# Performance work log

Measured on AMD Instinct MI355X. Metric: run time of the kernel, lower is better.

The kernel has to match this reference:

```python
import jax, jax.numpy as jnp
import numpy as np

INPUT_SIZE = 695 + 2 * 406 + 84  # 1591
HIDDEN = 1024
NUM_LAYERS = 2
B, T = 8, 2048


def _make_linear(key, fan_in, fan_out, forget_bias):
    kw, kb = jax.random.split(key)
    bound = 1.0 / np.sqrt(fan_in)
    W = jax.random.uniform(kw, (fan_in, fan_out), minval=-bound, maxval=bound, dtype=jnp.float32)
    b = jax.random.uniform(kb, (fan_out,), minval=-bound, maxval=bound, dtype=jnp.float32)
    H = fan_out // 3
    b = b.at[H:2 * H].set(forget_bias)  # init_input_passthrough: forget-gate bias = 6.0
    return W, b


def setup_inputs() -> dict:
    key = jax.random.key(0)
    k1, k2, k3, k4, k5 = jax.random.split(key, 5)
    prev_actions = jax.random.uniform(k1, (B, T, 695), dtype=jnp.float32)
    states = jax.random.uniform(k2, (B, T, 812), dtype=jnp.float32)
    metadata = jax.random.uniform(k3, (B, T, 84), dtype=jnp.float32)
    W1, b1 = _make_linear(k4, INPUT_SIZE, 3 * HIDDEN, 6.0)
    W2, b2 = _make_linear(k5, HIDDEN, 3 * HIDDEN, 6.0)
    return {"prev_actions": prev_actions, "states": states, "metadata": metadata,
            "W1": W1, "b1": b1, "W2": W2, "b2": b2}


def forget_mult(f, z):
    # c_t = f_t * z_t + (1 - f_t) * c_{t-1}, c_0 = 0; parallel (log-depth) scan over time.
    a = 1.0 - f          # decay
    b = f * z            # input term
    def combine(c1, c2):
        a1, b1 = c1
        a2, b2 = c2
        return a1 * a2, a2 * b1 + b2
    _, c = jax.lax.associative_scan(combine, (a, b), axis=-2)
    return c


def qrnn_layer(x, W, b):
    y = jnp.einsum('btd,dh->bth', x, W) + b          # [B,T,3H]
    Z, Fg, O = jnp.split(y, 3, axis=-1)
    C = forget_mult(jax.nn.sigmoid(Fg), jax.nn.relu(Z))  # [B,T,H]
    out = jax.nn.sigmoid(O) * C
    return out, C[..., -1, :]


def reference(prev_actions, states, metadata, W1, b1, W2, b2):
    x = jnp.concatenate([prev_actions, states, metadata], axis=-1)  # [B,T,1591]
    hs = []
    for W, b in ((W1, b1), (W2, b2)):
        x, h_last = qrnn_layer(x, W, b)
        hs.append(h_last)
    h = jnp.stack(hs, axis=-2)  # [B, num_layers, H]
    return x, h
```

## Files before the change

### kernel.cpp

```cpp
#include <hip/hip_runtime.h>

typedef unsigned short u16;
typedef unsigned int   u32;
typedef __attribute__((ext_vector_type(8))) short bf16x8;
typedef __attribute__((ext_vector_type(4))) float f32x4;
typedef __attribute__((ext_vector_type(2))) unsigned int u32x2;

#define B_ 8
#define T_ 2048
#define M_ 16384
#define N_ 3072
#define H_ 1024
#define L_ 32
#define NC_ 64

__device__ __forceinline__ u16 f2bf(float f) {
    union { float f; unsigned u; } v; v.f = f;
    unsigned r = v.u + 0x7FFFu + ((v.u >> 16) & 1u);
    return (u16)(r >> 16);
}
__device__ __forceinline__ float bf2f(u16 s) {
    union { unsigned u; float f; } v; v.u = ((unsigned)s) << 16;
    return v.f;
}
__device__ __forceinline__ float sigm(float x) {
    return 1.f / (1.f + __expf(-x));
}

__device__ __forceinline__ void gload_lds16(const void* g, void* l) {
    __builtin_amdgcn_global_load_lds(
        (const __attribute__((address_space(1))) unsigned int*)g,
        (__attribute__((address_space(3))) unsigned int*)l,
        16, 0, 0);
}

__device__ __forceinline__ float cc_el(int d, const float* pam, const float* stm,
                                       const float* mdm) {
    if (d < 695)  return pam[d];
    if (d < 1507) return stm[d - 695];
    if (d < 1591) return mdm[d - 1507];
    return 0.f;
}
__global__ void concat_cast(const float* __restrict__ pa, const float* __restrict__ st,
                            const float* __restrict__ md, u16* __restrict__ x) {
    const int m = blockIdx.x;
    const float* pam = pa + (size_t)m * 695;
    const float* stm = st + (size_t)m * 812;
    const float* mdm = md + (size_t)m * 84;
    u32* xm = (u32*)(x + (size_t)m * 1600);
    for (int d2 = threadIdx.x; d2 < 800; d2 += 256) {
        const float v0 = cc_el(d2 * 2,     pam, stm, mdm);
        const float v1 = cc_el(d2 * 2 + 1, pam, stm, mdm);
        xm[d2] = (u32)f2bf(v0) | ((u32)f2bf(v1) << 16);
    }
}

__global__ void wtrans(const float* __restrict__ W, u16* __restrict__ Wt, int K, int Kp) {
    __shared__ float tile[32][33];
    const int n0 = blockIdx.x << 5;
    const int k0 = blockIdx.y << 5;
    const int tx = threadIdx.x & 31, ty = threadIdx.x >> 5;
    #pragma unroll
    for (int i = 0; i < 32; i += 8) {
        int k = k0 + ty + i;
        tile[ty + i][tx] = (k < K) ? W[(size_t)k * N_ + n0 + tx] : 0.f;
    }
    __syncthreads();
    #pragma unroll
    for (int i = 0; i < 32; i += 8) {
        int n = n0 + ty + i;
        Wt[(size_t)n * Kp + k0 + tx] = f2bf(tile[tx][ty + i]);
    }
}

__global__ __launch_bounds__(512, 1)
void gemm8p(const u16* __restrict__ A, const u16* __restrict__ Bt,
            const float* __restrict__ bias, u16* __restrict__ Y,
            int Kp, int NK, int NBN) {
    __shared__ u16 lds[65536];
    const int tid = threadIdx.x;
    const int w = tid >> 6, l = tid & 63;
    const int wm = w >> 2, wn = w & 3;

    const int cpx = gridDim.x >> 3;
    const int xg = (blockIdx.x & 7) * cpx + (blockIdx.x >> 3);
    const int bm = xg / NBN, bn = xg % NBN;
    const int brow = bm << 8, bcol = bn << 8;

    const int srow = (w << 5) + (l >> 2);
    const int gslot = (l & 3) ^ ((l >> 3) & 3);
    const u16* ga = A  + (size_t)(brow + srow) * Kp + gslot * 8;
    const u16* gb = Bt + (size_t)(bcol + srow) * Kp + gslot * 8;
    const int ldst = w << 10;

    const int fl = ((l & 15) << 5) + ((((l >> 4) ^ ((l >> 1) & 3)) & 3) << 3);
    const int abase = wm << 12;
    const int bbase = 8192 + (wn << 11);

#define STG_A(r, kt) do {                                                      \
    gload_lds16(ga + (size_t)(kt) * 32,                   &lds[((r) << 14) + ldst]);        \
    gload_lds16(ga + (size_t)(kt) * 32 + 16 * (size_t)Kp, &lds[((r) << 14) + ldst + 512]);  \
} while (0)
#define STG_B(r, kt) do {                                                      \
    gload_lds16(gb + (size_t)(kt) * 32,                   &lds[((r) << 14) + 8192 + ldst]);       \
    gload_lds16(gb + (size_t)(kt) * 32 + 16 * (size_t)Kp, &lds[((r) << 14) + 8192 + ldst + 512]); \
} while (0)

    f32x4 acc[8][4] = {};

    STG_A(0, 0); STG_B(0, 0);
    STG_A(1, 1); STG_B(1, 1);
    STG_A(2, 2); STG_B(2, 2);
    asm volatile("s_waitcnt vmcnt(8)" ::: "memory");
    __builtin_amdgcn_s_barrier();
    asm volatile("" ::: "memory");

    for (int kt = 0; kt < NK; ++kt) {
        const int cur = kt & 3;
        const int nxt = (kt + 3 < NK) ? kt + 3 : kt;
        const int nb = (kt + 3) & 3;
        STG_A(nb, nxt);
        STG_B(nb, nxt);

        const int cb = cur << 14;
        bf16x8 bfr[4], af0[4], af1[4];
        #pragma unroll
        for (int ni = 0; ni < 4; ++ni)
            bfr[ni] = *reinterpret_cast<const bf16x8*>(&lds[cb + bbase + (ni << 9) + fl]);
        #pragma unroll
        for (int mi = 0; mi < 4; ++mi)
            af0[mi] = *reinterpret_cast<const bf16x8*>(&lds[cb + abase + (mi << 9) + fl]);
        #pragma unroll
        for (int mi = 0; mi < 4; ++mi)
            af1[mi] = *reinterpret_cast<const bf16x8*>(&lds[cb + abase + ((4 + mi) << 9) + fl]);

        #pragma unroll
        for (int mi = 0; mi < 4; ++mi)
            #pragma unroll
            for (int ni = 0; ni < 4; ++ni)
                acc[mi][ni] = __builtin_amdgcn_mfma_f32_16x16x32_bf16(
                    bfr[ni], af0[mi], acc[mi][ni], 0, 0, 0);
        #pragma unroll
        for (int mi = 0; mi < 4; ++mi)
            #pragma unroll
            for (int ni = 0; ni < 4; ++ni)
                acc[4 + mi][ni] = __builtin_amdgcn_mfma_f32_16x16x32_bf16(
                    bfr[ni], af1[mi], acc[4 + mi][ni], 0, 0, 0);

        asm volatile("s_waitcnt vmcnt(8)" ::: "memory");
        asm volatile("s_waitcnt lgkmcnt(0)" ::: "memory");
        __builtin_amdgcn_s_barrier();
        asm volatile("" ::: "memory");
    }

    asm volatile("s_waitcnt vmcnt(0)" ::: "memory");
    __builtin_amdgcn_s_barrier();

    const int nloc0 = (wn << 6) + ((l >> 4) << 2);
    float4 bv4[4];
    #pragma unroll
    for (int nf = 0; nf < 4; ++nf)
        bv4[nf] = *reinterpret_cast<const float4*>(&bias[bcol + nloc0 + nf * 16]);
    #pragma unroll
    for (int ci = 0; ci < 8; ++ci) {
        const int mrow = (wm << 7) + ((ci >> 2) << 6) + ((ci & 3) << 4) + (l & 15);
        #pragma unroll
        for (int nf = 0; nf < 4; ++nf) {
            const int nloc = nloc0 + nf * 16;
            u32x2 p;
            p.x = (u32)f2bf(acc[ci][nf][0] + bv4[nf].x) |
                  ((u32)f2bf(acc[ci][nf][1] + bv4[nf].y) << 16);
            p.y = (u32)f2bf(acc[ci][nf][2] + bv4[nf].z) |
                  ((u32)f2bf(acc[ci][nf][3] + bv4[nf].w) << 16);
            const int off = (mrow << 8) + (((nloc >> 3) ^ (mrow & 7)) << 3) +
                            ((nloc >> 2) & 1) * 4;
            *reinterpret_cast<u32x2*>(&lds[off]) = p;
        }
    }
    asm volatile("s_waitcnt lgkmcnt(0)" ::: "memory");
    __builtin_amdgcn_s_barrier();

    #pragma unroll
    for (int rp = 0; rp < 16; ++rp) {
        const int row = (w << 5) + (rp << 1) + (l >> 5);
        const int c16 = l & 31;
        const bf16x8 v = *reinterpret_cast<const bf16x8*>(
            &lds[(row << 8) + ((c16 ^ (row & 7)) << 3)]);
        *reinterpret_cast<bf16x8*>(&Y[(size_t)(brow + row) * N_ + bcol + c16 * 8]) = v;
    }
#undef STG_A
#undef STG_B
}

__global__ void scan_p1(const u16* __restrict__ y, float* __restrict__ aprod,
                        float* __restrict__ cend) {
    const int hb = blockIdx.x & 1;
    const int chunk = (blockIdx.x >> 1) & (NC_ - 1);
    const int b = blockIdx.x >> 7;
    const int h = (hb << 9) + (threadIdx.x << 1);
    const u16* yb = y + ((size_t)b * T_ + (size_t)chunk * L_) * N_;
    float a0 = 1.f, a1 = 1.f, c0 = 0.f, c1 = 0.f;
    #pragma unroll 4
    for (int t = 0; t < L_; ++t) {
        const u32 zz = *reinterpret_cast<const u32*>(&yb[t * N_ + h]);
        const u32 ff = *reinterpret_cast<const u32*>(&yb[t * N_ + H_ + h]);
        const float f0 = sigm(bf2f((u16)ff));
        const float f1 = sigm(bf2f((u16)(ff >> 16)));
        const float z0 = fmaxf(bf2f((u16)zz), 0.f);
        const float z1 = fmaxf(bf2f((u16)(zz >> 16)), 0.f);
        c0 = f0 * z0 + (1.f - f0) * c0;  a0 *= (1.f - f0);
        c1 = f1 * z1 + (1.f - f1) * c1;  a1 *= (1.f - f1);
    }
    const size_t idx = ((size_t)b * NC_ + chunk) * H_ + h;
    *reinterpret_cast<float2*>(&aprod[idx]) = make_float2(a0, a1);
    *reinterpret_cast<float2*>(&cend[idx])  = make_float2(c0, c1);
}

__global__ void scan_p2(const float* __restrict__ aprod, const float* __restrict__ cend,
                        float* __restrict__ cin, float* __restrict__ hout, int layer) {
    const int b = blockIdx.x >> 2;
    const int h = ((blockIdx.x & 3) << 8) + threadIdx.x;
    float c = 0.f;
    #pragma unroll
    for (int k = 0; k < NC_; ++k) {
        const size_t idx = ((size_t)b * NC_ + k) * H_ + h;
        cin[idx] = c;
        c = aprod[idx] * c + cend[idx];
    }
    hout[(size_t)(((b << 1) + layer) << 10) + h] = c;
}

__global__ void scan_p3(const u16* __restrict__ y, const float* __restrict__ cin,
                        void* __restrict__ xout, int layer) {
    const int hb = blockIdx.x & 1;
    const int chunk = (blockIdx.x >> 1) & (NC_ - 1);
    const int b = blockIdx.x >> 7;
    const int h = (hb << 9) + (threadIdx.x << 1);
    const u16* yb = y + ((size_t)b * T_ + (size_t)chunk * L_) * N_;
    const size_t cidx = ((size_t)b * NC_ + chunk) * H_ + h;
    const float2 cv = *reinterpret_cast<const float2*>(&cin[cidx]);
    float c0 = cv.x, c1 = cv.y;
    u32*    xo_bf = (u32*)xout;
    float2* xo_f  = (float2*)xout;
    const size_t obase = ((size_t)b * T_ + (size_t)chunk * L_) * H_ + h;
    #pragma unroll 4
    for (int t = 0; t < L_; ++t) {
        const u32 zz = *reinterpret_cast<const u32*>(&yb[t * N_ + h]);
        const u32 ff = *reinterpret_cast<const u32*>(&yb[t * N_ + H_ + h]);
        const u32 oo = *reinterpret_cast<const u32*>(&yb[t * N_ + 2 * H_ + h]);
        const float f0 = sigm(bf2f((u16)ff));
        const float f1 = sigm(bf2f((u16)(ff >> 16)));
        const float z0 = fmaxf(bf2f((u16)zz), 0.f);
        const float z1 = fmaxf(bf2f((u16)(zz >> 16)), 0.f);
        c0 = f0 * z0 + (1.f - f0) * c0;
        c1 = f1 * z1 + (1.f - f1) * c1;
        const float o0 = sigm(bf2f((u16)oo)) * c0;
        const float o1 = sigm(bf2f((u16)(oo >> 16))) * c1;
        const size_t oi = obase + (size_t)t * H_;
        if (layer) xo_f[oi >> 1] = make_float2(o0, o1);
        else       xo_bf[oi >> 1] = (u32)f2bf(o0) | ((u32)f2bf(o1) << 16);
    }
}

extern "C" void kernel_launch(void* const* d_in, const int* in_sizes, int n_in,
                              void* d_out, int out_size, void* d_ws, size_t ws_size,
                              hipStream_t stream) {
    const float* pa = (const float*)d_in[0];
    const float* st = (const float*)d_in[1];
    const float* md = (const float*)d_in[2];
    const float* W1 = (const float*)d_in[3];
    const float* b1 = (const float*)d_in[4];
    const float* W2 = (const float*)d_in[5];
    const float* b2 = (const float*)d_in[6];
    float* out = (float*)d_out;

    char* ws = (char*)d_ws;
    const size_t y_bytes = (size_t)M_ * N_ * 2;
    const size_t x_bytes = (size_t)M_ * 1600 * 2;
    u16* y  = (u16*)ws;
    u16* x  = (u16*)(ws + y_bytes);
    u16* Wt = (u16*)(ws + y_bytes + x_bytes);
    char* scr = ws + y_bytes + (size_t)M_ * H_ * 2;
    const size_t sarr = (size_t)B_ * NC_ * H_ * 4;
    float* aprod = (float*)scr;
    float* cend  = (float*)(scr + sarr);
    float* cin   = (float*)(scr + 2 * sarr);

    float* hout = out + (size_t)M_ * H_;

    const int grid_g = (M_ / 256) * (N_ / 256);

    concat_cast<<<M_, 256, 0, stream>>>(pa, st, md, x);
    wtrans<<<dim3(N_ / 32, 50), 256, 0, stream>>>(W1, Wt, 1591, 1600);
    gemm8p<<<grid_g, 512, 0, stream>>>(x, Wt, b1, y, 1600, 50, N_ / 256);
    scan_p1<<<B_ * NC_ * 2, 256, 0, stream>>>(y, aprod, cend);
    scan_p2<<<32, 256, 0, stream>>>(aprod, cend, cin, hout, 0);
    scan_p3<<<B_ * NC_ * 2, 256, 0, stream>>>(y, cin, x, 0);

    wtrans<<<dim3(N_ / 32, 32), 256, 0, stream>>>(W2, Wt, 1024, 1024);
    gemm8p<<<grid_g, 512, 0, stream>>>(x, Wt, b2, y, 1024, 32, N_ / 256);
    scan_p1<<<B_ * NC_ * 2, 256, 0, stream>>>(y, aprod, cend);
    scan_p2<<<32, 256, 0, stream>>>(aprod, cend, cin, hout, 1);
    scan_p3<<<B_ * NC_ * 2, 256, 0, stream>>>(y, cin, out, 1);
}
```

Baseline: 411.3 us.

## Use 4 waves per GEMM block with 128x128 per-wave tiles

The bf16 MFMA GEMM block shrinks from 8 waves to 4 waves while keeping the 256x256 block tile. Each wave now computes a 128x128 sub-tile (8x8 MFMA fragments) instead of 128x64, and issues four global-to-LDS loads per operand per k-step instead of two, with the wait counts adjusted to match. This raises register reuse of the LDS fragments and cuts LDS reads per MFMA, at the cost of doubling accumulator registers per thread and halving the number of waves available to hide latency.

```diff
diff --git a/kernel.cpp b/kernel.cpp
--- a/kernel.cpp
+++ b/kernel.cpp
@@ -73,45 +73,48 @@
     }
 }
 
-__global__ __launch_bounds__(512, 1)
+__global__ __launch_bounds__(256, 1)
 void gemm8p(const u16* __restrict__ A, const u16* __restrict__ Bt,
             const float* __restrict__ bias, u16* __restrict__ Y,
             int Kp, int NK, int NBN) {
     __shared__ u16 lds[65536];
     const int tid = threadIdx.x;
     const int w = tid >> 6, l = tid & 63;
-    const int wm = w >> 2, wn = w & 3;
+    const int wm = w >> 1, wn = w & 1;
 
     const int cpx = gridDim.x >> 3;
     const int xg = (blockIdx.x & 7) * cpx + (blockIdx.x >> 3);
     const int bm = xg / NBN, bn = xg % NBN;
     const int brow = bm << 8, bcol = bn << 8;
 
-    const int srow = (w << 5) + (l >> 2);
     const int gslot = (l & 3) ^ ((l >> 3) & 3);
-    const u16* ga = A  + (size_t)(brow + srow) * Kp + gslot * 8;
-    const u16* gb = Bt + (size_t)(bcol + srow) * Kp + gslot * 8;
-    const int ldst = w << 10;
+    const u16* ga = A  + (size_t)(brow + (w << 6) + (l >> 2)) * Kp + gslot * 8;
+    const u16* gb = Bt + (size_t)(bcol + (w << 6) + (l >> 2)) * Kp + gslot * 8;
+    const int ldst = w << 11;
 
     const int fl = ((l & 15) << 5) + ((((l >> 4) ^ ((l >> 1) & 3)) & 3) << 3);
     const int abase = wm << 12;
-    const int bbase = 8192 + (wn << 11);
-
-#define STG_A(r, kt) do {                                                      \
-    gload_lds16(ga + (size_t)(kt) * 32,                   &lds[((r) << 14) + ldst]);        \
-    gload_lds16(ga + (size_t)(kt) * 32 + 16 * (size_t)Kp, &lds[((r) << 14) + ldst + 512]);  \
+    const int bbase = 8192 + (wn << 12);
+
+#define STG_A(r, kt) do {                                                                    \
+    gload_lds16(ga + (size_t)(kt) * 32,                   &lds[((r) << 14) + ldst]);         \
+    gload_lds16(ga + (size_t)(kt) * 32 + 16 * (size_t)Kp, &lds[((r) << 14) + ldst + 512]);   \
+    gload_lds16(ga + (size_t)(kt) * 32 + 32 * (size_t)Kp, &lds[((r) << 14) + ldst + 1024]);  \
+    gload_lds16(ga + (size_t)(kt) * 32 + 48 * (size_t)Kp, &lds[((r) << 14) + ldst + 1536]);  \
 } while (0)
-#define STG_B(r, kt) do {                                                      \
-    gload_lds16(gb + (size_t)(kt) * 32,                   &lds[((r) << 14) + 8192 + ldst]);       \
-    gload_lds16(gb + (size_t)(kt) * 32 + 16 * (size_t)Kp, &lds[((r) << 14) + 8192 + ldst + 512]); \
+#define STG_B(r, kt) do {                                                                            \
+    gload_lds16(gb + (size_t)(kt) * 32,                   &lds[((r) << 14) + 8192 + ldst]);          \
+    gload_lds16(gb + (size_t)(kt) * 32 + 16 * (size_t)Kp, &lds[((r) << 14) + 8192 + ldst + 512]);    \
+    gload_lds16(gb + (size_t)(kt) * 32 + 32 * (size_t)Kp, &lds[((r) << 14) + 8192 + ldst + 1024]);   \
+    gload_lds16(gb + (size_t)(kt) * 32 + 48 * (size_t)Kp, &lds[((r) << 14) + 8192 + ldst + 1536]);   \
 } while (0)
 
-    f32x4 acc[8][4] = {};
+    f32x4 acc[8][8] = {};
 
     STG_A(0, 0); STG_B(0, 0);
     STG_A(1, 1); STG_B(1, 1);
     STG_A(2, 2); STG_B(2, 2);
-    asm volatile("s_waitcnt vmcnt(8)" ::: "memory");
+    asm volatile("s_waitcnt vmcnt(16)" ::: "memory");
     __builtin_amdgcn_s_barrier();
     asm volatile("" ::: "memory");
 
@@ -123,31 +126,22 @@
         STG_B(nb, nxt);
 
         const int cb = cur << 14;
-        bf16x8 bfr[4], af0[4], af1[4];
+        bf16x8 bfr[8], afr[8];
         #pragma unroll
-        for (int ni = 0; ni < 4; ++ni)
-            bfr[ni] = *reinterpret_cast<const bf16x8*>(&lds[cb + bbase + (ni << 9) + fl]);
+        for (int nf = 0; nf < 8; ++nf)
+            bfr[nf] = *reinterpret_cast<const bf16x8*>(&lds[cb + bbase + (nf << 9) + fl]);
         #pragma unroll
-        for (int mi = 0; mi < 4; ++mi)
-            af0[mi] = *reinterpret_cast<const bf16x8*>(&lds[cb + abase + (mi << 9) + fl]);
+        for (int mf = 0; mf < 8; ++mf)
+            afr[mf] = *reinterpret_cast<const bf16x8*>(&lds[cb + abase + (mf << 9) + fl]);
+
         #pragma unroll
-        for (int mi = 0; mi < 4; ++mi)
-            af1[mi] = *reinterpret_cast<const bf16x8*>(&lds[cb + abase + ((4 + mi) << 9) + fl]);
-
-        #pragma unroll
-        for (int mi = 0; mi < 4; ++mi)
+        for (int mf = 0; mf < 8; ++mf)
             #pragma unroll
-            for (int ni = 0; ni < 4; ++ni)
-                acc[mi][ni] = __builtin_amdgcn_mfma_f32_16x16x32_bf16(
-                    bfr[ni], af0[mi], acc[mi][ni], 0, 0, 0);
-        #pragma unroll
-        for (int mi = 0; mi < 4; ++mi)
-            #pragma unroll
-            for (int ni = 0; ni < 4; ++ni)
-                acc[4 + mi][ni] = __builtin_amdgcn_mfma_f32_16x16x32_bf16(
-                    bfr[ni], af1[mi], acc[4 + mi][ni], 0, 0, 0);
-
-        asm volatile("s_waitcnt vmcnt(8)" ::: "memory");
+            for (int nf = 0; nf < 8; ++nf)
+                acc[mf][nf] = __builtin_amdgcn_mfma_f32_16x16x32_bf16(
+                    bfr[nf], afr[mf], acc[mf][nf], 0, 0, 0);
+
+        asm volatile("s_waitcnt vmcnt(16)" ::: "memory");
         asm volatile("s_waitcnt lgkmcnt(0)" ::: "memory");
         __builtin_amdgcn_s_barrier();
         asm volatile("" ::: "memory");
@@ -156,22 +150,23 @@
     asm volatile("s_waitcnt vmcnt(0)" ::: "memory");
     __builtin_amdgcn_s_barrier();
 
-    const int nloc0 = (wn << 6) + ((l >> 4) << 2);
-    float4 bv4[4];
-    #pragma unroll
-    for (int nf = 0; nf < 4; ++nf)
-        bv4[nf] = *reinterpret_cast<const float4*>(&bias[bcol + nloc0 + nf * 16]);
-    #pragma unroll
-    for (int ci = 0; ci < 8; ++ci) {
-        const int mrow = (wm << 7) + ((ci >> 2) << 6) + ((ci & 3) << 4) + (l & 15);
+    const int nq = (l >> 4) << 2;
+    float4 bv4[8];
+    #pragma unroll
+    for (int nf = 0; nf < 8; ++nf)
+        bv4[nf] = *reinterpret_cast<const float4*>(
+            &bias[bcol + (wn << 7) + (nf << 4) + nq]);
+    #pragma unroll
+    for (int mf = 0; mf < 8; ++mf) {
+        const int mrow = (wm << 7) + (mf << 4) + (l & 15);
         #pragma unroll
-        for (int nf = 0; nf < 4; ++nf) {
-            const int nloc = nloc0 + nf * 16;
+        for (int nf = 0; nf < 8; ++nf) {
+            const int nloc = (wn << 7) + (nf << 4) + nq;
             u32x2 p;
-            p.x = (u32)f2bf(acc[ci][nf][0] + bv4[nf].x) |
-                  ((u32)f2bf(acc[ci][nf][1] + bv4[nf].y) << 16);
-            p.y = (u32)f2bf(acc[ci][nf][2] + bv4[nf].z) |
-                  ((u32)f2bf(acc[ci][nf][3] + bv4[nf].w) << 16);
+            p.x = (u32)f2bf(acc[mf][nf][0] + bv4[nf].x) |
+                  ((u32)f2bf(acc[mf][nf][1] + bv4[nf].y) << 16);
+            p.y = (u32)f2bf(acc[mf][nf][2] + bv4[nf].z) |
+                  ((u32)f2bf(acc[mf][nf][3] + bv4[nf].w) << 16);
             const int off = (mrow << 8) + (((nloc >> 3) ^ (mrow & 7)) << 3) +
                             ((nloc >> 2) & 1) * 4;
             *reinterpret_cast<u32x2*>(&lds[off]) = p;
@@ -181,8 +176,8 @@
     __builtin_amdgcn_s_barrier();
 
     #pragma unroll
-    for (int rp = 0; rp < 16; ++rp) {
-        const int row = (w << 5) + (rp << 1) + (l >> 5);
+    for (int rp = 0; rp < 32; ++rp) {
+        const int row = (w << 6) + (rp << 1) + (l >> 5);
         const int c16 = l & 31;
         const bf16x8 v = *reinterpret_cast<const bf16x8*>(
             &lds[(row << 8) + ((c16 ^ (row & 7)) << 3)]);
@@ -292,13 +287,13 @@
 
     concat_cast<<<M_, 256, 0, stream>>>(pa, st, md, x);
     wtrans<<<dim3(N_ / 32, 50), 256, 0, stream>>>(W1, Wt, 1591, 1600);
-    gemm8p<<<grid_g, 512, 0, stream>>>(x, Wt, b1, y, 1600, 50, N_ / 256);
+    gemm8p<<<grid_g, 256, 0, stream>>>(x, Wt, b1, y, 1600, 50, N_ / 256);
     scan_p1<<<B_ * NC_ * 2, 256, 0, stream>>>(y, aprod, cend);
     scan_p2<<<32, 256, 0, stream>>>(aprod, cend, cin, hout, 0);
     scan_p3<<<B_ * NC_ * 2, 256, 0, stream>>>(y, cin, x, 0);
 
     wtrans<<<dim3(N_ / 32, 32), 256, 0, stream>>>(W2, Wt, 1024, 1024);
-    gemm8p<<<grid_g, 512, 0, stream>>>(x, Wt, b2, y, 1024, 32, N_ / 256);
+    gemm8p<<<grid_g, 256, 0, stream>>>(x, Wt, b2, y, 1024, 32, N_ / 256);
     scan_p1<<<B_ * NC_ * 2, 256, 0, stream>>>(y, aprod, cend);
     scan_p2<<<32, 256, 0, stream>>>(aprod, cend, cin, hout, 1);
     scan_p3<<<B_ * NC_ * 2, 256, 0, stream>>>(y, cin, out, 1);
```

After: 426.3 us. 3.6% more time.
